# Performance work log

Hardware: AMD Instinct MI355X
Metric: run time of the kernel (lower is better)

## Reference

```python
import jax, jax.numpy as jnp
import numpy as np

NUM_USERS, NUM_ITEMS, DIM = 100000, 50000, 64
BATCH = 1024


def setup_inputs() -> dict:
    key = jax.random.key(0)
    k1, k2, k3, k4, k5, k6 = jax.random.split(key, 6)
    stdv = 1.0 / np.sqrt(DIM)
    return {
        "batch_users": jax.random.randint(k1, (BATCH,), 0, NUM_USERS),
        "whole_items": jnp.arange(NUM_ITEMS),
        "dropout_ration": 0,  # p=0 -> dropout is identity (deterministic reference)
        "user_table": 0.01 * jax.random.normal(k2, (NUM_USERS, DIM), dtype=jnp.float32),
        "item_table": 0.01 * jax.random.normal(k3, (NUM_ITEMS, DIM), dtype=jnp.float32),
        "weight_view": jax.random.uniform(k4, (DIM, 1), minval=-stdv, maxval=stdv, dtype=jnp.float32),
        "weight_cart": jax.random.uniform(k5, (DIM, 1), minval=-stdv, maxval=stdv, dtype=jnp.float32),
        "weight_buy": jax.random.uniform(k6, (DIM, 1), minval=-stdv, maxval=stdv, dtype=jnp.float32),
    }


def reference(batch_users, whole_items, dropout_ration, user_table, item_table,
              weight_view, weight_cart, weight_buy):
    # dropout with p=dropout_ration=0 is the identity
    u = user_table[batch_users]          # [B, D]
    v = item_table[whole_items]          # [I, D]
    # sum_d u[b,d] * v[i,d] * w[d]  ==  (u * w) @ v.T  -- never build [B,I,D]
    def score(w):
        return jnp.einsum('bd,id->bi', u * w[:, 0], v)
    likelihood_view = score(weight_view)
    likelihood_cart = score(weight_cart)
    likelihood_buy = score(weight_buy)
    return likelihood_view, likelihood_cart, likelihood_buy
```

## Files before the change

### kernel.cpp

```cpp
#include <hip/hip_runtime.h>


#define NUM_ITEMS 50000
#define NUM_B     1024
#define DIMK      64
#define ITILE     64
#define UC        32
#define VPAD      72
#define UPAD      72

typedef __bf16 bfrag_t __attribute__((ext_vector_type(8)));
typedef float  facc_t  __attribute__((ext_vector_type(4)));

__device__ __forceinline__ unsigned short f2bf(float f) {
    union { float f; unsigned u; } a; a.f = f;
    unsigned r = a.u + 0x7fffu + ((a.u >> 16) & 1u);
    return (unsigned short)(r >> 16);
}

__global__ __launch_bounds__(256) void gmf_kernel(
    const int*   __restrict__ users,
    const int*   __restrict__ items,
    const float* __restrict__ utab,
    const float* __restrict__ vtab,
    const float* __restrict__ wv,
    const float* __restrict__ wc,
    const float* __restrict__ wb,
    float*       __restrict__ out)
{
    __shared__ unsigned short vt[3][ITILE * VPAD];
    __shared__ unsigned short ut[UC * UPAD];

    const int t    = threadIdx.x;
    const int wave = t >> 6;
    const int lane = t & 63;
    const int quad = lane >> 4;
    const int l16  = lane & 15;
    const int iblk = blockIdx.x * ITILE;

    #pragma unroll
    for (int c = 0; c < 4; ++c) {
        int idx = t + 256 * c;
        int it  = idx >> 4;
        int f4  = idx & 15;
        int gi  = iblk + it;
        float4 v = make_float4(0.f, 0.f, 0.f, 0.f);
        if (gi < NUM_ITEMS) {
            int row = items[gi];
            v = *(const float4*)(vtab + row * DIMK + f4 * 4);
        }
        float4 w0 = *(const float4*)(wv + f4 * 4);
        float4 w1 = *(const float4*)(wc + f4 * 4);
        float4 w2 = *(const float4*)(wb + f4 * 4);
        ushort4 s;
        s.x = f2bf(v.x * w0.x); s.y = f2bf(v.y * w0.y);
        s.z = f2bf(v.z * w0.z); s.w = f2bf(v.w * w0.w);
        *(ushort4*)(&vt[0][it * VPAD + f4 * 4]) = s;
        s.x = f2bf(v.x * w1.x); s.y = f2bf(v.y * w1.y);
        s.z = f2bf(v.z * w1.z); s.w = f2bf(v.w * w1.w);
        *(ushort4*)(&vt[1][it * VPAD + f4 * 4]) = s;
        s.x = f2bf(v.x * w2.x); s.y = f2bf(v.y * w2.y);
        s.z = f2bf(v.z * w2.z); s.w = f2bf(v.w * w2.w);
        *(ushort4*)(&vt[2][it * VPAD + f4 * 4]) = s;
    }
    __syncthreads();

    bfrag_t bfx[3][2];
    #pragma unroll
    for (int x = 0; x < 3; ++x) {
        const unsigned short* vr = &vt[x][(wave * 16 + l16) * VPAD + quad * 8];
        bfx[x][0] = *(const bfrag_t*)(vr);
        bfx[x][1] = *(const bfrag_t*)(vr + 32);
    }

    const int  item   = iblk + wave * 16 + l16;
    const bool istore = (item < NUM_ITEMS);

    for (int uc = 0; uc < NUM_B / UC; ++uc) {
        __syncthreads();
        #pragma unroll
        for (int c = 0; c < 2; ++c) {
            int idx = t + 256 * c;
            int us  = idx >> 4;
            int f4  = idx & 15;
            int row = users[uc * UC + us];
            float4 u = *(const float4*)(utab + row * DIMK + f4 * 4);
            ushort4 s;
            s.x = f2bf(u.x); s.y = f2bf(u.y); s.z = f2bf(u.z); s.w = f2bf(u.w);
            *(ushort4*)(&ut[us * UPAD + f4 * 4]) = s;
        }
        __syncthreads();

        facc_t acc[2][3];
        #pragma unroll
        for (int s = 0; s < 2; ++s)
            #pragma unroll
            for (int x = 0; x < 3; ++x)
                acc[s][x] = (facc_t){0.f, 0.f, 0.f, 0.f};

        #pragma unroll
        for (int s = 0; s < 2; ++s) {
            const unsigned short* ur = &ut[(s * 16 + l16) * UPAD + quad * 8];
            bfrag_t a0 = *(const bfrag_t*)(ur);
            bfrag_t a1 = *(const bfrag_t*)(ur + 32);
            #pragma unroll
            for (int x = 0; x < 3; ++x) {
                acc[s][x] = __builtin_amdgcn_mfma_f32_16x16x32_bf16(a0, bfx[x][0], acc[s][x], 0, 0, 0);
                acc[s][x] = __builtin_amdgcn_mfma_f32_16x16x32_bf16(a1, bfx[x][1], acc[s][x], 0, 0, 0);
            }
        }

        if (istore) {
            #pragma unroll
            for (int x = 0; x < 3; ++x) {
                #pragma unroll
                for (int s = 0; s < 2; ++s) {
                    long b0 = uc * UC + s * 16 + quad * 4;
                    float* p = out + (long)x * NUM_B * NUM_ITEMS + b0 * NUM_ITEMS + item;
                    #pragma unroll
                    for (int r = 0; r < 4; ++r)
                        p[(long)r * NUM_ITEMS] = acc[s][x][r];
                }
            }
        }
    }
}

extern "C" void kernel_launch(void* const* d_in, const int* in_sizes, int n_in,
                              void* d_out, int out_size, void* d_ws, size_t ws_size,
                              hipStream_t stream) {
    const int*   users = (const int*)  d_in[0];
    const int*   items = (const int*)  d_in[1];
    const float* utab  = (const float*)d_in[3];
    const float* vtab  = (const float*)d_in[4];
    const float* wv    = (const float*)d_in[5];
    const float* wc    = (const float*)d_in[6];
    const float* wb    = (const float*)d_in[7];
    float* out = (float*)d_out;

    const int grid = (NUM_ITEMS + ITILE - 1) / ITILE;
    gmf_kernel<<<grid, 256, 0, stream>>>(users, items, utab, vtab, wv, wc, wb, out);
}
```

Before: 669.1 us.

## Load user rows directly into registers, swap MFMA operands for vectorized stores

Drops the shared-memory staging of user embeddings and the per-chunk barriers. Each lane now loads its user fragment straight from global memory into registers, with the next chunk prefetched while the current one computes. The MFMA operands are swapped so each lane holds four consecutive item columns, which lets outputs be written as 16-byte vector stores instead of scalar stores. This aims to cut sync overhead and widen the output writes, which dominate traffic, at the cost of more registers and redundant global loads of user rows across waves.

```diff
diff --git a/kernel.cpp b/kernel.cpp
--- a/kernel.cpp
+++ b/kernel.cpp
@@ -6,8 +6,8 @@
 #define DIMK      64
 #define ITILE     64
 #define UC        32
+#define NCHUNK    (NUM_B / UC)
 #define VPAD      72
-#define UPAD      72
 
 typedef __bf16 bfrag_t __attribute__((ext_vector_type(8)));
 typedef float  facc_t  __attribute__((ext_vector_type(4)));
@@ -16,6 +16,13 @@
     union { float f; unsigned u; } a; a.f = f;
     unsigned r = a.u + 0x7fffu + ((a.u >> 16) & 1u);
     return (unsigned short)(r >> 16);
+}
+
+__device__ __forceinline__ bfrag_t cvt8(float4 a, float4 b) {
+    bfrag_t r;
+    r[0] = (__bf16)a.x; r[1] = (__bf16)a.y; r[2] = (__bf16)a.z; r[3] = (__bf16)a.w;
+    r[4] = (__bf16)b.x; r[5] = (__bf16)b.y; r[6] = (__bf16)b.z; r[7] = (__bf16)b.w;
+    return r;
 }
 
 __global__ __launch_bounds__(256) void gmf_kernel(
@@ -29,7 +36,6 @@
     float*       __restrict__ out)
 {
     __shared__ unsigned short vt[3][ITILE * VPAD];
-    __shared__ unsigned short ut[UC * UPAD];
 
     const int t    = threadIdx.x;
     const int wave = t >> 6;
@@ -65,65 +71,83 @@
     }
     __syncthreads();
 
-    bfrag_t bfx[3][2];
+    bfrag_t vfx[3][2];
     #pragma unroll
     for (int x = 0; x < 3; ++x) {
         const unsigned short* vr = &vt[x][(wave * 16 + l16) * VPAD + quad * 8];
-        bfx[x][0] = *(const bfrag_t*)(vr);
-        bfx[x][1] = *(const bfrag_t*)(vr + 32);
+        vfx[x][0] = *(const bfrag_t*)(vr);
+        vfx[x][1] = *(const bfrag_t*)(vr + 32);
     }
 
-    const int  item   = iblk + wave * 16 + l16;
-    const bool istore = (item < NUM_ITEMS);
+    const int  icol   = iblk + wave * 16 + quad * 4;
+    const bool istore = (icol < NUM_ITEMS);
 
-    for (int uc = 0; uc < NUM_B / UC; ++uc) {
-        __syncthreads();
+    float* p[3][2];
+    #pragma unroll
+    for (int x = 0; x < 3; ++x)
         #pragma unroll
-        for (int c = 0; c < 2; ++c) {
-            int idx = t + 256 * c;
-            int us  = idx >> 4;
-            int f4  = idx & 15;
-            int row = users[uc * UC + us];
-            float4 u = *(const float4*)(utab + row * DIMK + f4 * 4);
-            ushort4 s;
-            s.x = f2bf(u.x); s.y = f2bf(u.y); s.z = f2bf(u.z); s.w = f2bf(u.w);
-            *(ushort4*)(&ut[us * UPAD + f4 * 4]) = s;
+        for (int s = 0; s < 2; ++s)
+            p[x][s] = out + ((long)x * NUM_B + s * 16 + l16) * (long)NUM_ITEMS + icol;
+
+    const float* ubase = utab + quad * 8;
+
+    auto loadu = [&](int uc, float4* r) {
+        #pragma unroll
+        for (int s = 0; s < 2; ++s) {
+            int row = users[uc * UC + s * 16 + l16];
+            const float* up = ubase + (long)row * DIMK;
+            r[s * 4 + 0] = *(const float4*)(up + 0);
+            r[s * 4 + 1] = *(const float4*)(up + 4);
+            r[s * 4 + 2] = *(const float4*)(up + 32);
+            r[s * 4 + 3] = *(const float4*)(up + 36);
         }
-        __syncthreads();
+    };
 
+    auto compute = [&](const float4* r) {
+        bfrag_t a[2][2];
+        #pragma unroll
+        for (int s = 0; s < 2; ++s) {
+            a[s][0] = cvt8(r[s * 4 + 0], r[s * 4 + 1]);
+            a[s][1] = cvt8(r[s * 4 + 2], r[s * 4 + 3]);
+        }
         facc_t acc[2][3];
         #pragma unroll
         for (int s = 0; s < 2; ++s)
             #pragma unroll
             for (int x = 0; x < 3; ++x)
                 acc[s][x] = (facc_t){0.f, 0.f, 0.f, 0.f};
-
         #pragma unroll
-        for (int s = 0; s < 2; ++s) {
-            const unsigned short* ur = &ut[(s * 16 + l16) * UPAD + quad * 8];
-            bfrag_t a0 = *(const bfrag_t*)(ur);
-            bfrag_t a1 = *(const bfrag_t*)(ur + 32);
+        for (int s = 0; s < 2; ++s)
             #pragma unroll
             for (int x = 0; x < 3; ++x) {
-                acc[s][x] = __builtin_amdgcn_mfma_f32_16x16x32_bf16(a0, bfx[x][0], acc[s][x], 0, 0, 0);
-                acc[s][x] = __builtin_amdgcn_mfma_f32_16x16x32_bf16(a1, bfx[x][1], acc[s][x], 0, 0, 0);
+                acc[s][x] = __builtin_amdgcn_mfma_f32_16x16x32_bf16(vfx[x][0], a[s][0], acc[s][x], 0, 0, 0);
+                acc[s][x] = __builtin_amdgcn_mfma_f32_16x16x32_bf16(vfx[x][1], a[s][1], acc[s][x], 0, 0, 0);
             }
-        }
-
         if (istore) {
             #pragma unroll
-            for (int x = 0; x < 3; ++x) {
+            for (int x = 0; x < 3; ++x)
                 #pragma unroll
-                for (int s = 0; s < 2; ++s) {
-                    long b0 = uc * UC + s * 16 + quad * 4;
-                    float* p = out + (long)x * NUM_B * NUM_ITEMS + b0 * NUM_ITEMS + item;
-                    #pragma unroll
-                    for (int r = 0; r < 4; ++r)
-                        p[(long)r * NUM_ITEMS] = acc[s][x][r];
-                }
-            }
+                for (int s = 0; s < 2; ++s)
+                    *(facc_t*)p[x][s] = acc[s][x];
         }
+        #pragma unroll
+        for (int x = 0; x < 3; ++x)
+            #pragma unroll
+            for (int s = 0; s < 2; ++s)
+                p[x][s] += (long)UC * NUM_ITEMS;
+    };
+
+    float4 raw[8];
+    loadu(0, raw);
+    #pragma unroll 4
+    for (int uc = 0; uc < NCHUNK - 1; ++uc) {
+        float4 nxt[8];
+        loadu(uc + 1, nxt);
+        compute(raw);
+        #pragma unroll
+        for (int i = 0; i < 8; ++i) raw[i] = nxt[i];
     }
+    compute(raw);
 }
 
 extern "C" void kernel_launch(void* const* d_in, const int* in_sizes, int n_in,
```

Measured after the change: 805.6 us. 1.2x slower.
